# Kernel tuning notes

Measured on AMD Instinct MI355X. Metric: run time of the kernel, lower is better.

The kernel has to match this reference:

```python
import math
import jax, jax.numpy as jnp
import numpy as np

# dims (match init_kwargs)
B, NMHC, T, D = 4, 4, 1024, 256
DK, DATTN, H, E = 16, 512, 8, 4
DV = DATTN // H          # 64
DKP = 2 * DK             # 32 (PoPE doubles d_key)
HE = H * E
R = max(DK // 4, 1)      # 4
DA = int(DK * 1.618)     # 25
DPG = max(int(DATTN * 0.618), 1)  # 316
ND = NMHC * D
EPS = 1e-6
ROUTE_TEMP = 1.0

def _rms(x):
    return x * jax.lax.rsqrt(jnp.mean(x * x, axis=-1, keepdims=True) + EPS)

def _sinkhorn(M, n_iters=6):
    M = jnp.exp(M)
    for _ in range(n_iters):
        M = M / jnp.sum(M, axis=-1, keepdims=True)
        M = M / jnp.sum(M, axis=-2, keepdims=True)
    return M

def _l2norm(x):
    return x / jnp.maximum(jnp.linalg.norm(x, axis=-1, keepdims=True), 1e-12)

def _pope(x, phi):
    mu = jax.nn.softplus(x)
    return jnp.concatenate([mu * jnp.cos(phi), mu * jnp.sin(phi)], axis=-1)

def setup_inputs() -> dict:
    key = jax.random.key(0)
    ks = iter(jax.random.split(key, 40))
    rn = lambda shape, s=0.02: jax.random.normal(next(ks), shape, jnp.float32) * s
    return {
        'stream': jax.random.normal(next(ks), (B, NMHC, T, D), jnp.float32),
        'Wq': rn((H, D, DK)), 'Wk': rn((H, D, DK)), 'Wv': rn((H, D, DV)),
        'pope_delta': rn((DK,), 0.1),
        'q_router': rn((H, D, E), 0.05), 'kv_router': rn((H, D, E), 0.05),
        'lora_A_q': rn((HE, D, R), 0.01), 'lora_B_q': rn((HE, R, DK)),
        'lora_A_k': rn((HE, D, R), 0.01), 'lora_B_k': rn((HE, R, DK)),
        'lora_A_v': rn((HE, D, R), 0.01), 'lora_B_v': rn((HE, R, DV)),
        'alpha_up': rn((HE, D, DA), 0.01), 'alpha_down': rn((HE, DA, DKP), 0.01),
        'beta_up': rn((HE, D, DA), 0.01), 'beta_down': rn((HE, DA, 1), 0.01),
        'mhc_norm_w': jnp.ones((HE, ND)),
        'phi_pre': rn((HE, ND, NMHC)), 'phi_post': rn((HE, ND, NMHC)),
        'phi_res': rn((HE, ND, NMHC * NMHC)),
        'b_pre': jnp.zeros((HE, NMHC)), 'b_post': jnp.zeros((HE, NMHC)),
        'b_res': jnp.zeros((HE, NMHC, NMHC)),
        'a_pre': jnp.ones((HE,)), 'a_post': jnp.ones((HE,)), 'a_res': jnp.ones((HE,)),
        'norm_w': jnp.ones((HE, D)),
        'W_pre': rn((HE, D, DATTN), 0.01),
        'W_o': rn((DATTN, D)),
        'W_pg1': rn((HE, D, DPG), 0.01), 'W_pg2': rn((HE, DPG, D), 0.01),
    }

def _forward(stream, Wq, Wk, Wv, pope_delta, q_router, kv_router,
             lora_A_q, lora_B_q, lora_A_k, lora_B_k, lora_A_v, lora_B_v,
             alpha_up, alpha_down, beta_up, beta_down,
             mhc_norm_w, phi_pre, phi_post, phi_res, b_pre, b_post, b_res,
             a_pre, a_post, a_res, norm_w, W_pre, W_o, W_pg1, W_pg2):
    dt = stream.dtype
    freqs = 10000.0 ** (jnp.arange(DK, dtype=dt) / DK)
    pos = jnp.arange(T, dtype=dt)
    phi_q = pos[:, None] * freqs[None, :]                       # (T,DK)
    phi_k = phi_q - 2.0 * math.pi * jax.nn.sigmoid(pope_delta)  # key phase shift

    # MHC RMSNorm has no bias; fold its per-expert weight into the phi matrices
    x_hat = _rms(jnp.reshape(jnp.swapaxes(stream, 1, 2), (B, T, ND)))
    route_in = jnp.mean(stream, axis=1)                         # (B,T,D)

    q_logits = jnp.clip(jnp.einsum('btd,hde->hbte', route_in, q_router), -10, 10)
    q_probs = jax.nn.softmax(q_logits / ROUTE_TEMP, axis=-1)
    q_sel = jnp.argmax(q_logits, axis=-1)                       # (H,B,T) eval-mode routing
    kv_logits = jnp.clip(jnp.einsum('btd,hde->hbte', route_in, kv_router), -10, 10)
    kv_probs = jax.nn.softmax(kv_logits / ROUTE_TEMP, axis=-1)
    kv_sel = jnp.argmax(kv_logits, axis=-1)
    eidx = jnp.arange(E)

    acc_pre = jnp.zeros((B, T, H * DV), dt)
    acc_post = jnp.zeros((B, T, D), dt)
    acc_res = jnp.zeros((B, T, NMHC, NMHC), dt)
    acc_hpost = jnp.zeros((B, T, NMHC), dt)
    outs = []
    for h in range(H):
        s = slice(h * E, (h + 1) * E)
        nw = mhc_norm_w[s][:, :, None]
        Hpre = jax.nn.sigmoid(a_pre[s][:, None, None, None] * jnp.einsum('btk,ekn->ebtn', x_hat, nw * phi_pre[s]) + b_pre[s][:, None, None, :])
        Hpost = 2.0 * jax.nn.sigmoid(a_post[s][:, None, None, None] * jnp.einsum('btk,ekn->ebtn', x_hat, nw * phi_post[s]) + b_post[s][:, None, None, :])
        res_l = jnp.einsum('btk,ekm->ebtm', x_hat, nw * phi_res[s]).reshape(E, B, T, NMHC, NMHC)
        Hres = _sinkhorn(a_res[s][:, None, None, None, None] * res_l + b_res[s][:, None, None, :, :])

        he = jnp.einsum('ebtn,bntd->ebtd', Hpre, stream)        # (E,B,T,D)
        he = _rms(he) * norm_w[s][:, None, None, :]

        # straight-through routing weights (forward == hard mask)
        qp = jnp.moveaxis(q_probs[h], -1, 0)[..., None]         # (E,B,T,1)
        qm = (q_sel[h][None] == eidx[:, None, None]).astype(dt)[..., None]
        eff_q = qp + jax.lax.stop_gradient(qm - qp)
        kp = jnp.moveaxis(kv_probs[h], -1, 0)[..., None]
        km = (kv_sel[h][None] == eidx[:, None, None]).astype(dt)[..., None]
        eff_kv = kp + jax.lax.stop_gradient(km - kp)

        # Q path (expert 0 is a no-op for Q)
        dq = jnp.einsum('ebtr,erk->ebtk', jax.nn.silu(jnp.einsum('ebtd,edr->ebtr', he, lora_A_q[s])), lora_B_q[s])
        q_e = _pope(_l2norm(jnp.einsum('ebtd,dk->ebtk', he, Wq[h]) + dq), phi_q)
        pg = jax.nn.sigmoid(jnp.einsum('ebtp,epd->ebtd', jax.nn.silu(jnp.einsum('ebtd,edp->ebtp', he, W_pg1[s])), W_pg2[s]))
        q_h = jnp.sum(eff_q[1:] * q_e[1:], axis=0)
        acc_post = acc_post + jnp.sum(eff_q[1:] * pg[1:], axis=0) / H

        # KV path (all experts)
        dk_ = jnp.einsum('ebtr,erk->ebtk', jax.nn.silu(jnp.einsum('ebtd,edr->ebtr', he, lora_A_k[s])), lora_B_k[s])
        k_e = _pope(_l2norm(jnp.einsum('ebtd,dk->ebtk', he, Wk[h]) + dk_), phi_k)
        dv_ = jnp.einsum('ebtr,erk->ebtk', jax.nn.silu(jnp.einsum('ebtd,edr->ebtr', he, lora_A_v[s])), lora_B_v[s])
        v_e = jax.nn.silu(jnp.einsum('ebtd,dk->ebtk', he, Wv[h]) + dv_)
        al_e = jax.nn.sigmoid(jnp.einsum('ebta,eak->ebtk', jax.nn.silu(jnp.einsum('ebtd,eda->ebta', he, alpha_up[s])), alpha_down[s]))
        be_e = jax.nn.sigmoid(jnp.einsum('ebta,eak->ebtk', jax.nn.silu(jnp.einsum('ebtd,eda->ebta', he, beta_up[s])), beta_down[s]))
        preg = jax.nn.silu(jnp.einsum('ebtd,edc->ebtc', he, W_pre[s]))
        k_h = jnp.sum(eff_kv * k_e, axis=0)
        v_h = jnp.sum(eff_kv * v_e, axis=0)
        al_h = jnp.sum(eff_kv * al_e, axis=0)
        be_h = jnp.sum(eff_kv * be_e, axis=0)
        acc_pre = acc_pre + jnp.sum(eff_kv * preg, axis=0) / H
        acc_res = acc_res + jnp.sum(Hres * eff_kv[..., None], axis=0)
        acc_hpost = acc_hpost + jnp.sum(Hpost * eff_kv, axis=0)

        # KDA delta-rule recurrence over T (state S: (B,DKP,DV))
        def step(S, inp):
            q_t, k_t, v_t, a_t, b_t = inp
            aS = a_t[:, :, None] * S
            kaS = jnp.einsum('bd,bde->be', k_t, aS)
            S_new = aS + b_t[:, :, None] * (k_t[:, :, None] * (v_t - kaS)[:, None, :])
            return S_new, jnp.einsum('bd,bde->be', q_t, S_new)
        xs = tuple(jnp.swapaxes(a, 0, 1) for a in (q_h, k_h, v_h, al_h, be_h))
        _, o = jax.lax.scan(step, jnp.zeros((B, DKP, DV), dt), xs)
        out_h = jnp.where((q_sel[h] == 0)[..., None], jnp.zeros((), dt), jnp.swapaxes(o, 0, 1))
        outs.append(out_h)

    concat = jnp.concatenate(outs, axis=-1) / math.sqrt(H * DV)
    result = (concat * acc_pre) @ W_o * acc_post                # (B,T,D)
    res = jnp.einsum('btij,bjtd->bitd', acc_res / H, stream)    # stream mixing
    return res + jnp.einsum('btn,btd->bntd', acc_hpost / H, result)

def reference(stream, Wq, Wk, Wv, pope_delta, q_router, kv_router,
              lora_A_q, lora_B_q, lora_A_k, lora_B_k, lora_A_v, lora_B_v,
              alpha_up, alpha_down, beta_up, beta_down,
              mhc_norm_w, phi_pre, phi_post, phi_res, b_pre, b_post, b_res,
              a_pre, a_post, a_res, norm_w, W_pre, W_o, W_pg1, W_pg2):
    return _forward(stream, Wq, Wk, Wv, pope_delta, q_router, kv_router,
                    lora_A_q, lora_B_q, lora_A_k, lora_B_k, lora_A_v, lora_B_v,
                    alpha_up, alpha_down, beta_up, beta_down,
                    mhc_norm_w, phi_pre, phi_post, phi_res, b_pre, b_post, b_res,
                    a_pre, a_post, a_res, norm_w, W_pre, W_o, W_pg1, W_pg2)
```

## Files before the change

kernel.cpp:

```cpp
#include <hip/hip_runtime.h>
#include <math.h>

#define B_ 4
#define NM 4
#define T_ 1024
#define D_ 256
#define DK_ 16
#define DV_ 64
#define DKP_ 32
#define H_ 8
#define E_ 4
#define HE_ 32
#define R_ 4
#define DA_ 25
#define DPG_ 316
#define ND_ 1024
#define DATTN_ 512
#define BT_ 4096
#define TB 16
#define TT 64

#define OFF_CNT     0
#define OFF_ACCPRE  256
#define OFF_ACCPOST (OFF_ACCPRE + BT_*512)
#define OFF_ACCRES  (OFF_ACCPOST + BT_*256)
#define OFF_ACCHP   (OFF_ACCRES + BT_*16)
#define OFF_QH      (OFF_ACCHP + BT_*4)
#define ZERO_END    (OFF_QH + H_*BT_*32)
#define OFF_KH      ZERO_END
#define OFF_VH      (OFF_KH + H_*BT_*32)
#define OFF_ALH     (OFF_VH + H_*BT_*64)
#define OFF_BEH     (OFF_ALH + H_*BT_*32)
#define OFF_LKV     (OFF_BEH + H_*BT_)
#define OFF_LQ      (OFF_LKV + HE_*BT_)
#define OFF_RMS     (OFF_LQ + HE_*BT_)
#define OFF_ATTN    (OFF_RMS + BT_)
#define OFF_TRIG    (OFF_ATTN + BT_*512)
#define WS_FLOATS   (OFF_TRIG + 4*T_*DK_)

__device__ __forceinline__ float sigf(float x){ return 1.0f/(1.0f+expf(-x)); }
__device__ __forceinline__ float siluf(float x){ return x/(1.0f+expf(-x)); }
__device__ __forceinline__ float softplusf(float x){ return fmaxf(x,0.0f)+log1pf(expf(-fabsf(x))); }

__global__ __launch_bounds__(256) void k_trig(const float* __restrict__ delta, float* __restrict__ ws){
  int idx = blockIdx.x*256 + threadIdx.x;
  int t = idx >> 4, k = idx & 15;
  double fr = pow(10000.0, (double)k / 16.0);
  float freq = (float)fr;
  float pq = (float)t * freq;
  float sg = sigf(delta[k]);
  float shift = (float)(2.0*M_PI) * sg;
  float pk = pq - shift;
  float* tr = ws + OFF_TRIG;
  tr[idx]         = (float)cos((double)pq);
  tr[16384+idx]   = (float)sin((double)pq);
  tr[32768+idx]   = (float)cos((double)pk);
  tr[49152+idx]   = (float)sin((double)pk);
}

__global__ __launch_bounds__(256) void k_route(const float* __restrict__ stream,
    const float* __restrict__ q_router, const float* __restrict__ kv_router,
    float* __restrict__ ws){
  __shared__ float s_route[256];
  __shared__ float s_red[4];
  __shared__ float s_log[64];
  int tok = blockIdx.x; int b = tok >> 10, t = tok & 1023;
  int d = threadIdx.x;
  const float* sp = stream + ((size_t)(b*4)*1024 + t)*256 + d;
  float s0 = sp[0];
  float s1 = sp[1024*256];
  float s2 = sp[2*1024*256];
  float s3 = sp[3*1024*256];
  s_route[d] = (((s0+s1)+s2)+s3)*0.25f;
  float ssp = s0*s0+s1*s1+s2*s2+s3*s3;
  for (int off=32; off; off>>=1) ssp += __shfl_xor(ssp, off, 64);
  if ((d & 63)==0) s_red[d>>6] = ssp;
  __syncthreads();
  if (d==0){
    float ss = ((s_red[0]+s_red[1])+s_red[2])+s_red[3];
    float mean = ss*(1.0f/1024.0f) + 1e-6f;
    ws[OFF_RMS + tok] = (float)(1.0/sqrt((double)mean));
  }
  if (d < 64){
    int lane = d;
    int r = lane>>5, h = (lane>>2)&7, e = lane&3;
    const float* R = (r ? kv_router : q_router) + h*1024 + e;
    float acc = 0.f;
    for (int dd=0; dd<256; ++dd) acc = fmaf(s_route[dd], R[dd*4], acc);
    s_log[lane] = fminf(fmaxf(acc,-10.f),10.f);
  }
  if (d < 16){
    int r = d>>3, h = d&7;
    int base = r*32 + h*4;
    int best=0; float bv = s_log[base];
    for (int e=1;e<4;e++){ float v=s_log[base+e]; if (v>bv){bv=v;best=e;} }
    int* cnt = (int*)ws;
    if (r==1){
      int* lst = (int*)(ws + OFF_LKV);
      int pos = atomicAdd(&cnt[h*4+best],1);
      lst[(h*4+best)*BT_ + pos] = tok;
    } else if (best>0){
      int* lst = (int*)(ws + OFF_LQ);
      int pos = atomicAdd(&cnt[32 + h*4+best],1);
      lst[(h*4+best)*BT_ + pos] = tok;
    }
  }
}

__global__ __launch_bounds__(256) void k_expert_kv(
    const float* __restrict__ stream, float* ws,
    const float* __restrict__ Wk, const float* __restrict__ Wv,
    const float* __restrict__ lora_A_k, const float* __restrict__ lora_B_k,
    const float* __restrict__ lora_A_v, const float* __restrict__ lora_B_v,
    const float* __restrict__ alpha_up, const float* __restrict__ alpha_down,
    const float* __restrict__ beta_up, const float* __restrict__ beta_down,
    const float* __restrict__ mhc_norm_w, const float* __restrict__ phi_pre,
    const float* __restrict__ phi_post, const float* __restrict__ phi_res,
    const float* __restrict__ b_pre, const float* __restrict__ b_post, const float* __restrict__ b_res,
    const float* __restrict__ a_pre, const float* __restrict__ a_post, const float* __restrict__ a_res,
    const float* __restrict__ norm_w, const float* __restrict__ W_pre)
{
  int g = blockIdx.y; int h = g>>2;
  const int* cnt = (const int*)ws;
  int c = cnt[g];
  int start = blockIdx.x*TB;
  if (start >= c) return;
  int nact = min(TB, c-start);

  __shared__ float s_he[TB][256];
  __shared__ float s_nw[1024];
  __shared__ float s_gnw[256];
  __shared__ float s_lrk[TB][4];
  __shared__ float s_lrv[TB][4];
  __shared__ float s_au[TB][25];
  __shared__ float s_bu[TB][25];
  __shared__ int s_tok[TB];
  int tid = threadIdx.x;
  if (tid < TB) s_tok[tid] = (tid < nact) ? ((const int*)(ws + OFF_LKV))[g*BT_ + start + tid] : -1;
  for (int i=tid;i<1024;i+=256) s_nw[i] = mhc_norm_w[g*1024+i];
  s_gnw[tid] = norm_w[g*256+tid];
  __syncthreads();

  float aP = a_pre[g], aQ = a_post[g], aR = a_res[g];
  int hw = tid>>5, lane = tid&31;

  for (int ii=0; ii<2; ++ii){
    int ti = hw + ii*8;
    int tok = s_tok[ti];
    if (tok < 0){
      #pragma unroll
      for (int m=0;m<8;++m) s_he[ti][m*32+lane] = 0.f;
      continue;
    }
    int b = tok>>10, t = tok&1023;
    const float* sb = stream + ((size_t)b*4*1024 + (size_t)t)*256;
    float rms = ws[OFF_RMS + tok];
    const float4* ppre  = (const float4*)(phi_pre  + (size_t)g*4096);
    const float4* ppost = (const float4*)(phi_post + (size_t)g*4096);
    const float4* pres  = (const float4*)(phi_res  + (size_t)g*16384);
    float dA[24];
    #pragma unroll
    for (int n=0;n<24;++n) dA[n]=0.f;
    #pragma unroll 2
    for (int j=0;j<32;++j){
      int k = j*32 + lane;
      float xv = sb[(size_t)(k>>8)*262144 + (k&255)] * rms * s_nw[k];
      float4 pa = ppre[k];
      float4 pb = ppost[k];
      float4 r0 = pres[4*k+0], r1 = pres[4*k+1], r2 = pres[4*k+2], r3 = pres[4*k+3];
      dA[0]=fmaf(xv,pa.x,dA[0]);  dA[1]=fmaf(xv,pa.y,dA[1]);  dA[2]=fmaf(xv,pa.z,dA[2]);  dA[3]=fmaf(xv,pa.w,dA[3]);
      dA[4]=fmaf(xv,pb.x,dA[4]);  dA[5]=fmaf(xv,pb.y,dA[5]);  dA[6]=fmaf(xv,pb.z,dA[6]);  dA[7]=fmaf(xv,pb.w,dA[7]);
      dA[8]=fmaf(xv,r0.x,dA[8]);  dA[9]=fmaf(xv,r0.y,dA[9]);  dA[10]=fmaf(xv,r0.z,dA[10]); dA[11]=fmaf(xv,r0.w,dA[11]);
      dA[12]=fmaf(xv,r1.x,dA[12]); dA[13]=fmaf(xv,r1.y,dA[13]); dA[14]=fmaf(xv,r1.z,dA[14]); dA[15]=fmaf(xv,r1.w,dA[15]);
      dA[16]=fmaf(xv,r2.x,dA[16]); dA[17]=fmaf(xv,r2.y,dA[17]); dA[18]=fmaf(xv,r2.z,dA[18]); dA[19]=fmaf(xv,r2.w,dA[19]);
      dA[20]=fmaf(xv,r3.x,dA[20]); dA[21]=fmaf(xv,r3.y,dA[21]); dA[22]=fmaf(xv,r3.z,dA[22]); dA[23]=fmaf(xv,r3.w,dA[23]);
    }
    #pragma unroll
    for (int n=0;n<24;++n){
      float v = dA[n];
      v += __shfl_xor(v,16,32); v += __shfl_xor(v,8,32); v += __shfl_xor(v,4,32);
      v += __shfl_xor(v,2,32);  v += __shfl_xor(v,1,32);
      dA[n]=v;
    }
    float g0 = sigf(aP*dA[0]+b_pre[g*4+0]);
    float g1 = sigf(aP*dA[1]+b_pre[g*4+1]);
    float g2 = sigf(aP*dA[2]+b_pre[g*4+2]);
    float g3 = sigf(aP*dA[3]+b_pre[g*4+3]);
    if (lane>=16 && lane<20){
      int n = lane-16;
      float hp = 2.f*sigf(aQ*dA[4+n] + b_post[g*4+n]);
      unsafeAtomicAdd(ws + OFF_ACCHP + tok*4 + n, hp);
    }
    if (lane<16){
      float m = expf(aR*dA[8+lane] + b_res[g*16+lane]);
      for (int itr=0; itr<6; ++itr){
        float rsum = m;
        rsum += __shfl_xor(rsum, 1, 4);
        rsum += __shfl_xor(rsum, 2, 4);
        m = m / rsum;
        float csum = m;
        csum += __shfl_xor(csum, 4, 16);
        csum += __shfl_xor(csum, 8, 16);
        m = m / csum;
      }
      unsafeAtomicAdd(ws + OFF_ACCRES + tok*16 + lane, m);
    }
    float he[8]; float ssp = 0.f;
    #pragma unroll
    for (int m=0;m<8;++m){
      int d = m*32+lane;
      float hv = fmaf(g3, sb[3*262144+d], fmaf(g2, sb[2*262144+d], fmaf(g1, sb[262144+d], g0*sb[d])));
      he[m]=hv; ssp = fmaf(hv,hv,ssp);
    }
    ssp += __shfl_xor(ssp,16,32); ssp += __shfl_xor(ssp,8,32); ssp += __shfl_xor(ssp,4,32);
    ssp += __shfl_xor(ssp,2,32);  ssp += __shfl_xor(ssp,1,32);
    float scale = (float)(1.0/sqrt((double)(ssp*(1.0f/256.0f)+1e-6f)));
    #pragma unroll
    for (int m=0;m<8;++m){
      int d = m*32+lane;
      s_he[ti][d] = he[m]*scale*s_gnw[d];
    }
  }
  __syncthreads();

  if (tid < 128){
    int tt = (tid & 63) >> 2, r = tid & 3;
    const float* A = (tid < 64 ? lora_A_k : lora_A_v) + g*1024 + r;
    float acc = 0.f;
    for (int dd=0; dd<256; ++dd) acc = fmaf(s_he[tt][dd], A[dd*4], acc);
    float sv = siluf(acc);
    if (tid<64) s_lrk[tt][r] = sv; else s_lrv[tt][r] = sv;
  }
  __syncthreads();
  {
    int tt = tid>>4, kk = tid&15;
    float acc=0.f;
    const float* Wkp = Wk + h*4096 + kk;
    for (int dd=0; dd<256; ++dd) acc = fmaf(s_he[tt][dd], Wkp[dd*16], acc);
    float dkv = 0.f;
    for (int r=0;r<4;r++) dkv = fmaf(s_lrk[tt][r], lora_B_k[g*64 + r*16 + kk], dkv);
    acc += dkv;
    float ssq = acc*acc;
    ssq += __shfl_xor(ssq, 1, 16);
    ssq += __shfl_xor(ssq, 2, 16);
    ssq += __shfl_xor(ssq, 4, 16);
    ssq += __shfl_xor(ssq, 8, 16);
    float den = fmaxf(sqrtf(ssq), 1e-12f);
    float xn = acc/den;
    float mu = softplusf(xn);
    if (tt < nact){
      int tok = s_tok[tt]; int t = tok&1023;
      float* kh = ws + OFF_KH + ((size_t)h*BT_ + tok)*32;
      const float* ck = ws + OFF_TRIG + 32768;
      const float* sk = ws + OFF_TRIG + 49152;
      kh[kk]    = mu*ck[t*16+kk];
      kh[16+kk] = mu*sk[t*16+kk];
    }
  }
  for (int pass=0; pass<4; ++pass){
    int tt = pass*4 + (tid>>6), col = tid&63;
    float acc=0.f;
    const float* Wvp = Wv + h*16384 + col;
    for (int dd=0; dd<256; ++dd) acc = fmaf(s_he[tt][dd], Wvp[dd*64], acc);
    for (int r=0;r<4;r++) acc = fmaf(s_lrv[tt][r], lora_B_v[g*256 + r*64 + col], acc);
    if (tt < nact)
      ws[OFF_VH + ((size_t)h*BT_ + s_tok[tt])*64 + col] = siluf(acc);
  }
  for (int idx = tid; idx < nact*25; idx += 256){
    int tt = idx/25, aa = idx%25;
    const float* Au = alpha_up + g*6400 + aa;
    float acc=0.f;
    for (int dd=0; dd<256; ++dd) acc = fmaf(s_he[tt][dd], Au[dd*25], acc);
    s_au[tt][aa] = siluf(acc);
    const float* Bu = beta_up + g*6400 + aa;
    float acc2=0.f;
    for (int dd=0; dd<256; ++dd) acc2 = fmaf(s_he[tt][dd], Bu[dd*25], acc2);
    s_bu[tt][aa] = siluf(acc2);
  }
  __syncthreads();
  for (int idx = tid; idx < nact*32; idx += 256){
    int tt = idx>>5, kk = idx&31;
    float acc=0.f;
    for (int aa=0; aa<25; ++aa) acc = fmaf(s_au[tt][aa], alpha_down[g*800 + aa*32 + kk], acc);
    ws[OFF_ALH + ((size_t)h*BT_ + s_tok[tt])*32 + kk] = sigf(acc);
  }
  if (tid < nact){
    float acc=0.f;
    for (int aa=0; aa<25; ++aa) acc = fmaf(s_bu[tid][aa], beta_down[g*25+aa], acc);
    ws[OFF_BEH + (size_t)h*BT_ + s_tok[tid]] = sigf(acc);
  }
  {
    float acc0[TB], acc1[TB];
    #pragma unroll
    for (int tt=0;tt<TB;++tt){acc0[tt]=0.f;acc1[tt]=0.f;}
    const float* Wp = W_pre + (size_t)g*131072;
    for (int dd=0; dd<256; ++dd){
      float w0 = Wp[dd*512 + tid];
      float w1 = Wp[dd*512 + 256 + tid];
      #pragma unroll
      for (int tt=0;tt<TB;++tt){
        float hvv = s_he[tt][dd];
        acc0[tt] = fmaf(hvv, w0, acc0[tt]);
        acc1[tt] = fmaf(hvv, w1, acc1[tt]);
      }
    }
    for (int tt=0;tt<nact;++tt){
      int tok = s_tok[tt];
      unsafeAtomicAdd(ws + OFF_ACCPRE + (size_t)tok*512 + tid,       siluf(acc0[tt]));
      unsafeAtomicAdd(ws + OFF_ACCPRE + (size_t)tok*512 + 256 + tid, siluf(acc1[tt]));
    }
  }
}

__global__ __launch_bounds__(256) void k_expert_q(
    const float* __restrict__ stream, float* ws,
    const float* __restrict__ Wq, const float* __restrict__ lora_A_q, const float* __restrict__ lora_B_q,
    const float* __restrict__ mhc_norm_w, const float* __restrict__ phi_pre,
    const float* __restrict__ b_pre, const float* __restrict__ a_pre,
    const float* __restrict__ norm_w, const float* __restrict__ W_pg1, const float* __restrict__ W_pg2)
{
  int g = blockIdx.y; int h = g>>2;
  const int* cnt = (const int*)ws;
  int c = cnt[32+g];
  int start = blockIdx.x*TB;
  if (start >= c) return;
  int nact = min(TB, c-start);

  __shared__ float s_he[TB][256];
  __shared__ float s_u[TB][DPG_];
  __shared__ float s_nw[1024];
  __shared__ float s_gnw[256];
  __shared__ float s_lrq[TB][4];
  __shared__ int s_tok[TB];
  int tid = threadIdx.x;
  if (tid < TB) s_tok[tid] = (tid<nact) ? ((const int*)(ws + OFF_LQ))[g*BT_ + start + tid] : -1;
  for (int i=tid;i<1024;i+=256) s_nw[i] = mhc_norm_w[g*1024+i];
  s_gnw[tid] = norm_w[g*256+tid];
  __syncthreads();
  float aP = a_pre[g];
  int hw = tid>>5, lane = tid&31;

  for (int ii=0; ii<2; ++ii){
    int ti = hw + ii*8;
    int tok = s_tok[ti];
    if (tok < 0){
      #pragma unroll
      for (int m=0;m<8;++m) s_he[ti][m*32+lane] = 0.f;
      continue;
    }
    int b = tok>>10, t = tok&1023;
    const float* sb = stream + ((size_t)b*4*1024 + (size_t)t)*256;
    float rms = ws[OFF_RMS + tok];
    const float4* ppre = (const float4*)(phi_pre + (size_t)g*4096);
    float d0=0.f,d1=0.f,d2=0.f,d3=0.f;
    #pragma unroll 4
    for (int j=0;j<32;++j){
      int k = j*32 + lane;
      float xv = sb[(size_t)(k>>8)*262144 + (k&255)] * rms * s_nw[k];
      float4 pa = ppre[k];
      d0=fmaf(xv,pa.x,d0); d1=fmaf(xv,pa.y,d1); d2=fmaf(xv,pa.z,d2); d3=fmaf(xv,pa.w,d3);
    }
    d0 += __shfl_xor(d0,16,32); d0 += __shfl_xor(d0,8,32); d0 += __shfl_xor(d0,4,32); d0 += __shfl_xor(d0,2,32); d0 += __shfl_xor(d0,1,32);
    d1 += __shfl_xor(d1,16,32); d1 += __shfl_xor(d1,8,32); d1 += __shfl_xor(d1,4,32); d1 += __shfl_xor(d1,2,32); d1 += __shfl_xor(d1,1,32);
    d2 += __shfl_xor(d2,16,32); d2 += __shfl_xor(d2,8,32); d2 += __shfl_xor(d2,4,32); d2 += __shfl_xor(d2,2,32); d2 += __shfl_xor(d2,1,32);
    d3 += __shfl_xor(d3,16,32); d3 += __shfl_xor(d3,8,32); d3 += __shfl_xor(d3,4,32); d3 += __shfl_xor(d3,2,32); d3 += __shfl_xor(d3,1,32);
    float g0 = sigf(aP*d0+b_pre[g*4+0]);
    float g1 = sigf(aP*d1+b_pre[g*4+1]);
    float g2 = sigf(aP*d2+b_pre[g*4+2]);
    float g3 = sigf(aP*d3+b_pre[g*4+3]);
    float he[8]; float ssp = 0.f;
    #pragma unroll
    for (int m=0;m<8;++m){
      int d = m*32+lane;
      float hv = fmaf(g3, sb[3*262144+d], fmaf(g2, sb[2*262144+d], fmaf(g1, sb[262144+d], g0*sb[d])));
      he[m]=hv; ssp = fmaf(hv,hv,ssp);
    }
    ssp += __shfl_xor(ssp,16,32); ssp += __shfl_xor(ssp,8,32); ssp += __shfl_xor(ssp,4,32);
    ssp += __shfl_xor(ssp,2,32);  ssp += __shfl_xor(ssp,1,32);
    float scale = (float)(1.0/sqrt((double)(ssp*(1.0f/256.0f)+1e-6f)));
    #pragma unroll
    for (int m=0;m<8;++m){
      int d = m*32+lane;
      s_he[ti][d] = he[m]*scale*s_gnw[d];
    }
  }
  __syncthreads();

  if (tid<64){
    int tt=tid>>2, r=tid&3;
    const float* A = lora_A_q + g*1024 + r;
    float acc=0.f;
    for (int dd=0;dd<256;++dd) acc = fmaf(s_he[tt][dd], A[dd*4], acc);
    s_lrq[tt][r] = siluf(acc);
  }
  __syncthreads();
  {
    int tt=tid>>4, kk=tid&15;
    const float* Wqp = Wq + h*4096 + kk;
    float acc=0.f;
    for (int dd=0;dd<256;++dd) acc = fmaf(s_he[tt][dd], Wqp[dd*16], acc);
    float dq=0.f;
    for (int r=0;r<4;r++) dq = fmaf(s_lrq[tt][r], lora_B_q[g*64+r*16+kk], dq);
    acc += dq;
    float ssq = acc*acc;
    ssq += __shfl_xor(ssq,1,16); ssq += __shfl_xor(ssq,2,16);
    ssq += __shfl_xor(ssq,4,16); ssq += __shfl_xor(ssq,8,16);
    float den = fmaxf(sqrtf(ssq),1e-12f);
    float xn = acc/den;
    float mu = softplusf(xn);
    if (tt<nact){
      int tok=s_tok[tt]; int t=tok&1023;
      float* qh = ws + OFF_QH + ((size_t)h*BT_+tok)*32;
      const float* cq = ws + OFF_TRIG;
      const float* sq = ws + OFF_TRIG + 16384;
      qh[kk]    = mu*cq[t*16+kk];
      qh[16+kk] = mu*sq[t*16+kk];
    }
  }
  for (int pb=0; pb<2; ++pb){
    int p = pb*256 + tid;
    if (p < DPG_){
      float accq[TB];
      #pragma unroll
      for (int tt=0;tt<TB;++tt) accq[tt]=0.f;
      const float* Wp = W_pg1 + (size_t)g*80896 + p;
      for (int dd=0;dd<256;++dd){
        float w = Wp[(size_t)dd*316];
        #pragma unroll
        for (int tt=0;tt<TB;++tt) accq[tt] = fmaf(s_he[tt][dd], w, accq[tt]);
      }
      #pragma unroll
      for (int tt=0;tt<TB;++tt) s_u[tt][p] = siluf(accq[tt]);
    }
  }
  __syncthreads();
  {
    float acc2[TB];
    #pragma unroll
    for (int tt=0;tt<TB;++tt) acc2[tt]=0.f;
    const float* Wp2 = W_pg2 + (size_t)g*80896 + tid;
    for (int p=0;p<DPG_;++p){
      float w = Wp2[(size_t)p*256];
      #pragma unroll
      for (int tt=0;tt<TB;++tt) acc2[tt] = fmaf(s_u[tt][p], w, acc2[tt]);
    }
    for (int tt=0;tt<nact;++tt)
      unsafeAtomicAdd(ws + OFF_ACCPOST + (size_t)s_tok[tt]*256 + tid, sigf(acc2[tt]));
  }
}

__global__ __launch_bounds__(256) void k_kda(float* ws){
  int hb = blockIdx.x; int h = hb>>2, b = hb&3;
  int tid = threadIdx.x;
  int e = tid >> 2, dg = tid & 3;
  const float* qb = ws + OFF_QH  + ((size_t)h*BT_ + b*T_)*32;
  const float* kb = ws + OFF_KH  + ((size_t)h*BT_ + b*T_)*32;
  const float* ab = ws + OFF_ALH + ((size_t)h*BT_ + b*T_)*32;
  const float* vb = ws + OFF_VH  + ((size_t)h*BT_ + b*T_)*64;
  const float* bb = ws + OFF_BEH + (size_t)h*BT_ + b*T_;
  float* ob = ws + OFF_ATTN + (size_t)b*T_*512 + h*64;

  __shared__ float s_q[TT*32];
  __shared__ float s_k[TT*32];
  __shared__ float s_a[TT*32];
  __shared__ float s_v[TT*64];
  __shared__ float s_b[TT];
  __shared__ float s_o[TT*64];

  float S[8];
  #pragma unroll
  for (int j=0;j<8;++j) S[j]=0.f;

  for (int t0=0; t0<T_; t0+=TT){
    {
      const float4* q4 = (const float4*)(qb + t0*32);
      const float4* k4 = (const float4*)(kb + t0*32);
      const float4* a4 = (const float4*)(ab + t0*32);
      const float4* v4 = (const float4*)(vb + t0*64);
      #pragma unroll
      for (int r=0;r<2;++r){
        int i = r*256 + tid;
        ((float4*)s_q)[i] = q4[i];
        ((float4*)s_k)[i] = k4[i];
        ((float4*)s_a)[i] = a4[i];
      }
      #pragma unroll
      for (int r=0;r<4;++r){
        int i = r*256 + tid;
        ((float4*)s_v)[i] = v4[i];
      }
      if (tid < TT) s_b[tid] = bb[t0+tid];
    }
    __syncthreads();
    #pragma unroll 4
    for (int tt=0; tt<TT; ++tt){
      const float* kp = s_k + tt*32 + dg*8;
      const float* ap = s_a + tt*32 + dg*8;
      const float* qp = s_q + tt*32 + dg*8;
      float v  = s_v[tt*64 + e];
      float be = s_b[tt];
      float part = 0.f;
      float kv[8], av[8];
      #pragma unroll
      for (int j=0;j<8;++j){ kv[j]=kp[j]; av[j]=ap[j]; part = fmaf(kv[j]*av[j], S[j], part); }
      part += __shfl_xor(part, 1, 4);
      part += __shfl_xor(part, 2, 4);
      float w = be*(v - part);
      float op = 0.f;
      #pragma unroll
      for (int j=0;j<8;++j){
        S[j] = fmaf(w, kv[j], av[j]*S[j]);
        op = fmaf(qp[j], S[j], op);
      }
      op += __shfl_xor(op, 1, 4);
      op += __shfl_xor(op, 2, 4);
      if (dg==0) s_o[tt*64 + e] = op / 22.627416997969522f;
    }
    __syncthreads();
    for (int i=tid; i<TT*16; i+=256){
      int tt = i>>4, c = i&15;
      ((float4*)(ob + (size_t)(t0+tt)*512))[c] = ((const float4*)(s_o + tt*64))[c];
    }
  }
}

__global__ __launch_bounds__(256) void k_final(const float* __restrict__ stream,
    const float* __restrict__ W_o, float* ws, float* __restrict__ out){
  __shared__ float s_m[8][512];
  __shared__ float s_rs[8][16];
  __shared__ float s_hp[8][4];
  int tid = threadIdx.x;
  int t0 = blockIdx.x*8;
  for (int tt=0;tt<8;++tt){
    int tok = t0+tt;
    for (int idx=tid; idx<512; idx+=256)
      s_m[tt][idx] = ws[OFF_ATTN + (size_t)tok*512 + idx] * (0.125f*ws[OFF_ACCPRE + (size_t)tok*512 + idx]);
    if (tid<16) s_rs[tt][tid] = 0.125f*ws[OFF_ACCRES + tok*16 + tid];
    if (tid<4)  s_hp[tt][tid] = 0.125f*ws[OFF_ACCHP + tok*4 + tid];
  }
  __syncthreads();
  float facc[8];
  #pragma unroll
  for (int tt=0;tt<8;++tt) facc[tt]=0.f;
  const float* Wop = W_o + tid;
  for (int cc=0;cc<512;++cc){
    float w = Wop[(size_t)cc*256];
    #pragma unroll
    for (int tt=0;tt<8;++tt) facc[tt] = fmaf(s_m[tt][cc], w, facc[tt]);
  }
  for (int tt=0;tt<8;++tt){
    int tok=t0+tt; int b=tok>>10, t=tok&1023;
    float result = facc[tt]*(0.125f*ws[OFF_ACCPOST + (size_t)tok*256 + tid]);
    float st[4];
    #pragma unroll
    for (int j=0;j<4;++j) st[j]=stream[(((size_t)b*4+j)*1024+t)*256+tid];
    #pragma unroll
    for (int n=0;n<4;++n){
      float rv = fmaf(s_rs[tt][n*4+3], st[3],
                 fmaf(s_rs[tt][n*4+2], st[2],
                 fmaf(s_rs[tt][n*4+1], st[1], s_rs[tt][n*4]*st[0])));
      out[(((size_t)b*4+n)*1024+t)*256+tid] = rv + s_hp[tt][n]*result;
    }
  }
}

extern "C" void kernel_launch(void* const* d_in, const int* in_sizes, int n_in,
                              void* d_out, int out_size, void* d_ws, size_t ws_size,
                              hipStream_t stream){
  const float* s = (const float*)d_in[0];
  float* ws = (float*)d_ws;
  hipMemsetAsync(d_ws, 0, (size_t)ZERO_END*4, stream);
  k_trig<<<64,256,0,stream>>>((const float*)d_in[4], ws);
  k_route<<<4096,256,0,stream>>>(s, (const float*)d_in[5], (const float*)d_in[6], ws);
  dim3 g2(BT_/TB, 32);
  k_expert_kv<<<g2,256,0,stream>>>(s, ws,
      (const float*)d_in[2],  (const float*)d_in[3],
      (const float*)d_in[9],  (const float*)d_in[10],
      (const float*)d_in[11], (const float*)d_in[12],
      (const float*)d_in[13], (const float*)d_in[14],
      (const float*)d_in[15], (const float*)d_in[16],
      (const float*)d_in[17], (const float*)d_in[18],
      (const float*)d_in[19], (const float*)d_in[20],
      (const float*)d_in[21], (const float*)d_in[22], (const float*)d_in[23],
      (const float*)d_in[24], (const float*)d_in[25], (const float*)d_in[26],
      (const float*)d_in[27], (const float*)d_in[28]);
  k_expert_q<<<g2,256,0,stream>>>(s, ws,
      (const float*)d_in[1],  (const float*)d_in[7], (const float*)d_in[8],
      (const float*)d_in[17], (const float*)d_in[18],
      (const float*)d_in[21], (const float*)d_in[24],
      (const float*)d_in[27], (const float*)d_in[30], (const float*)d_in[31]);
  k_kda<<<32,256,0,stream>>>(ws);
  k_final<<<512,256,0,stream>>>(s, (const float*)d_in[29], ws, (float*)d_out);
}
```

Baseline: 1.544 ms.

## Stage phi weights in shared memory and merge W_pg1 passes

In the K/V expert kernel, the phi_pre/post/res projection weights are now cooperatively staged into shared memory in 128-column chunks. Each warp computes the 24 dot products for its two tokens together, so every weight is read once per block instead of once per token and rereads from global/L2 are avoided. In the Q expert kernel, the two W_pg1 column passes are merged into one loop that reuses each s_he value for two outputs. s_he rows are also padded to reduce bank conflicts. This adds more syncthreads, LDS usage and register pressure, which can lower occupancy.

```diff
diff --git a/kernel.cpp b/kernel.cpp
--- a/kernel.cpp
+++ b/kernel.cpp
@@ -127,7 +127,9 @@
   if (start >= c) return;
   int nact = min(TB, c-start);
 
-  __shared__ float s_he[TB][256];
+  __shared__ float s_he[TB][258];
+  __shared__ float s_phi[24][128];
+  __shared__ float s_dots[TB][24];
   __shared__ float s_nw[1024];
   __shared__ float s_gnw[256];
   __shared__ float s_lrk[TB][4];
@@ -143,56 +145,77 @@
 
   float aP = a_pre[g], aQ = a_post[g], aR = a_res[g];
   int hw = tid>>5, lane = tid&31;
-
-  for (int ii=0; ii<2; ++ii){
-    int ti = hw + ii*8;
-    int tok = s_tok[ti];
+  int ti0 = hw, ti1 = hw+8;
+  int tok0 = s_tok[ti0], tok1 = s_tok[ti1];
+  const float* sb0 = stream + (tok0>=0 ? ((size_t)(tok0>>10)*4*262144 + (size_t)(tok0&1023)*256) : 0);
+  const float* sb1 = stream + (tok1>=0 ? ((size_t)(tok1>>10)*4*262144 + (size_t)(tok1&1023)*256) : 0);
+  float rn0 = (tok0>=0) ? ws[OFF_RMS + tok0] : 0.f;
+  float rn1 = (tok1>=0) ? ws[OFF_RMS + tok1] : 0.f;
+
+  float dA0[24], dA1[24];
+  #pragma unroll
+  for (int n=0;n<24;++n){ dA0[n]=0.f; dA1[n]=0.f; }
+  for (int cc=0; cc<8; ++cc){
+    __syncthreads();
+    {
+      int kk = tid & 127;
+      int np = tid >> 7;
+      int kg = cc*128 + kk;
+      #pragma unroll
+      for (int it=0; it<12; ++it){
+        int n = np + it*2;
+        float v;
+        if (n < 4)       v = phi_pre [(size_t)g*4096  + (size_t)kg*4  + n];
+        else if (n < 8)  v = phi_post[(size_t)g*4096  + (size_t)kg*4  + (n-4)];
+        else             v = phi_res [(size_t)g*16384 + (size_t)kg*16 + (n-8)];
+        s_phi[n][kk] = v;
+      }
+    }
+    __syncthreads();
+    int rr = cc>>1;
+    int off = (cc&1)*128 + lane*4;
+    float4 x0 = *(const float4*)(sb0 + (size_t)rr*262144 + off);
+    float4 x1 = *(const float4*)(sb1 + (size_t)rr*262144 + off);
+    float4 nw4 = *(const float4*)(&s_nw[cc*128 + lane*4]);
+    x0.x *= rn0*nw4.x; x0.y *= rn0*nw4.y; x0.z *= rn0*nw4.z; x0.w *= rn0*nw4.w;
+    x1.x *= rn1*nw4.x; x1.y *= rn1*nw4.y; x1.z *= rn1*nw4.z; x1.w *= rn1*nw4.w;
+    #pragma unroll
+    for (int n=0;n<24;++n){
+      float4 p4 = *(const float4*)(&s_phi[n][lane*4]);
+      dA0[n] = fmaf(x0.w,p4.w,fmaf(x0.z,p4.z,fmaf(x0.y,p4.y,fmaf(x0.x,p4.x,dA0[n]))));
+      dA1[n] = fmaf(x1.w,p4.w,fmaf(x1.z,p4.z,fmaf(x1.y,p4.y,fmaf(x1.x,p4.x,dA1[n]))));
+    }
+  }
+  #pragma unroll
+  for (int n=0;n<24;++n){
+    float v0=dA0[n], v1=dA1[n];
+    v0 += __shfl_xor(v0,16,32); v0 += __shfl_xor(v0,8,32); v0 += __shfl_xor(v0,4,32); v0 += __shfl_xor(v0,2,32); v0 += __shfl_xor(v0,1,32);
+    v1 += __shfl_xor(v1,16,32); v1 += __shfl_xor(v1,8,32); v1 += __shfl_xor(v1,4,32); v1 += __shfl_xor(v1,2,32); v1 += __shfl_xor(v1,1,32);
+    dA0[n]=v0; dA1[n]=v1;
+  }
+  float bp0=b_pre[g*4+0], bp1=b_pre[g*4+1], bp2=b_pre[g*4+2], bp3=b_pre[g*4+3];
+
+  auto finish = [&](int ti, int tok, const float (&dAx)[24], const float* sbx){
     if (tok < 0){
       #pragma unroll
       for (int m=0;m<8;++m) s_he[ti][m*32+lane] = 0.f;
-      continue;
-    }
-    int b = tok>>10, t = tok&1023;
-    const float* sb = stream + ((size_t)b*4*1024 + (size_t)t)*256;
-    float rms = ws[OFF_RMS + tok];
-    const float4* ppre  = (const float4*)(phi_pre  + (size_t)g*4096);
-    const float4* ppost = (const float4*)(phi_post + (size_t)g*4096);
-    const float4* pres  = (const float4*)(phi_res  + (size_t)g*16384);
-    float dA[24];
-    #pragma unroll
-    for (int n=0;n<24;++n) dA[n]=0.f;
-    #pragma unroll 2
-    for (int j=0;j<32;++j){
-      int k = j*32 + lane;
-      float xv = sb[(size_t)(k>>8)*262144 + (k&255)] * rms * s_nw[k];
-      float4 pa = ppre[k];
-      float4 pb = ppost[k];
-      float4 r0 = pres[4*k+0], r1 = pres[4*k+1], r2 = pres[4*k+2], r3 = pres[4*k+3];
-      dA[0]=fmaf(xv,pa.x,dA[0]);  dA[1]=fmaf(xv,pa.y,dA[1]);  dA[2]=fmaf(xv,pa.z,dA[2]);  dA[3]=fmaf(xv,pa.w,dA[3]);
-      dA[4]=fmaf(xv,pb.x,dA[4]);  dA[5]=fmaf(xv,pb.y,dA[5]);  dA[6]=fmaf(xv,pb.z,dA[6]);  dA[7]=fmaf(xv,pb.w,dA[7]);
-      dA[8]=fmaf(xv,r0.x,dA[8]);  dA[9]=fmaf(xv,r0.y,dA[9]);  dA[10]=fmaf(xv,r0.z,dA[10]); dA[11]=fmaf(xv,r0.w,dA[11]);
-      dA[12]=fmaf(xv,r1.x,dA[12]); dA[13]=fmaf(xv,r1.y,dA[13]); dA[14]=fmaf(xv,r1.z,dA[14]); dA[15]=fmaf(xv,r1.w,dA[15]);
-      dA[16]=fmaf(xv,r2.x,dA[16]); dA[17]=fmaf(xv,r2.y,dA[17]); dA[18]=fmaf(xv,r2.z,dA[18]); dA[19]=fmaf(xv,r2.w,dA[19]);
-      dA[20]=fmaf(xv,r3.x,dA[20]); dA[21]=fmaf(xv,r3.y,dA[21]); dA[22]=fmaf(xv,r3.z,dA[22]); dA[23]=fmaf(xv,r3.w,dA[23]);
-    }
-    #pragma unroll
-    for (int n=0;n<24;++n){
-      float v = dA[n];
-      v += __shfl_xor(v,16,32); v += __shfl_xor(v,8,32); v += __shfl_xor(v,4,32);
-      v += __shfl_xor(v,2,32);  v += __shfl_xor(v,1,32);
-      dA[n]=v;
-    }
-    float g0 = sigf(aP*dA[0]+b_pre[g*4+0]);
-    float g1 = sigf(aP*dA[1]+b_pre[g*4+1]);
-    float g2 = sigf(aP*dA[2]+b_pre[g*4+2]);
-    float g3 = sigf(aP*dA[3]+b_pre[g*4+3]);
+      return;
+    }
+    if (lane==0){
+      #pragma unroll
+      for (int n=0;n<24;++n) s_dots[ti][n] = dAx[n];
+    }
+    float g0 = sigf(aP*dAx[0]+bp0);
+    float g1 = sigf(aP*dAx[1]+bp1);
+    float g2 = sigf(aP*dAx[2]+bp2);
+    float g3 = sigf(aP*dAx[3]+bp3);
     if (lane>=16 && lane<20){
       int n = lane-16;
-      float hp = 2.f*sigf(aQ*dA[4+n] + b_post[g*4+n]);
+      float hp = 2.f*sigf(aQ*s_dots[ti][4+n] + b_post[g*4+n]);
       unsafeAtomicAdd(ws + OFF_ACCHP + tok*4 + n, hp);
     }
     if (lane<16){
-      float m = expf(aR*dA[8+lane] + b_res[g*16+lane]);
+      float m = expf(aR*s_dots[ti][8+lane] + b_res[g*16+lane]);
       for (int itr=0; itr<6; ++itr){
         float rsum = m;
         rsum += __shfl_xor(rsum, 1, 4);
@@ -209,7 +232,7 @@
     #pragma unroll
     for (int m=0;m<8;++m){
       int d = m*32+lane;
-      float hv = fmaf(g3, sb[3*262144+d], fmaf(g2, sb[2*262144+d], fmaf(g1, sb[262144+d], g0*sb[d])));
+      float hv = fmaf(g3, sbx[3*262144+d], fmaf(g2, sbx[2*262144+d], fmaf(g1, sbx[262144+d], g0*sbx[d])));
       he[m]=hv; ssp = fmaf(hv,hv,ssp);
     }
     ssp += __shfl_xor(ssp,16,32); ssp += __shfl_xor(ssp,8,32); ssp += __shfl_xor(ssp,4,32);
@@ -220,7 +243,9 @@
       int d = m*32+lane;
       s_he[ti][d] = he[m]*scale*s_gnw[d];
     }
-  }
+  };
+  finish(ti0, tok0, dA0, sb0);
+  finish(ti1, tok1, dA1, sb1);
   __syncthreads();
 
   if (tid < 128){
@@ -326,7 +351,7 @@
   if (start >= c) return;
   int nact = min(TB, c-start);
 
-  __shared__ float s_he[TB][256];
+  __shared__ float s_he[TB][258];
   __shared__ float s_u[TB][DPG_];
   __shared__ float s_nw[1024];
   __shared__ float s_gnw[256];
@@ -417,20 +442,29 @@
       qh[16+kk] = mu*sq[t*16+kk];
     }
   }
-  for (int pb=0; pb<2; ++pb){
-    int p = pb*256 + tid;
-    if (p < DPG_){
-      float accq[TB];
-      #pragma unroll
-      for (int tt=0;tt<TB;++tt) accq[tt]=0.f;
-      const float* Wp = W_pg1 + (size_t)g*80896 + p;
-      for (int dd=0;dd<256;++dd){
-        float w = Wp[(size_t)dd*316];
-        #pragma unroll
-        for (int tt=0;tt<TB;++tt) accq[tt] = fmaf(s_he[tt][dd], w, accq[tt]);
+  {
+    float accq[TB], accq2[TB];
+    #pragma unroll
+    for (int tt=0;tt<TB;++tt){ accq[tt]=0.f; accq2[tt]=0.f; }
+    int p = tid;
+    int p2 = 256 + tid;
+    bool has2 = (p2 < DPG_);
+    const float* Wp  = W_pg1 + (size_t)g*80896 + p;
+    const float* Wp2 = W_pg1 + (size_t)g*80896 + (has2 ? p2 : p);
+    for (int dd=0;dd<256;++dd){
+      float w  = Wp [(size_t)dd*316];
+      float w2 = Wp2[(size_t)dd*316];
+      #pragma unroll
+      for (int tt=0;tt<TB;++tt){
+        float hvv = s_he[tt][dd];
+        accq[tt]  = fmaf(hvv, w,  accq[tt]);
+        accq2[tt] = fmaf(hvv, w2, accq2[tt]);
       }
-      #pragma unroll
-      for (int tt=0;tt<TB;++tt) s_u[tt][p] = siluf(accq[tt]);
+    }
+    #pragma unroll
+    for (int tt=0;tt<TB;++tt){
+      s_u[tt][p] = siluf(accq[tt]);
+      if (has2) s_u[tt][p2] = siluf(accq2[tt]);
     }
   }
   __syncthreads();
```

After: 1.509 ms. -2.2%, faster.
